# Kernel optimization log

Measured on AMD Instinct MI355X. Metric: run time of the kernel, lower is better.

The kernel has to match this reference:

```python
import jax, jax.numpy as jnp
import numpy as np

DIM = 2048; N_HEADS = 16; Q_RANK = 1536; KV_RANK = 192
NOPE = 128; ROPE = 64; QK_HD = NOPE + ROPE  # 192 == KV_RANK (required by k_norm/cache widths)
B = 2; S = 2048; MAX_SEQ = 2048
EPS = 1e-6
SCALE = QK_HD ** -0.5


def _rms(v, w):
    return v * jax.lax.rsqrt(jnp.mean(v * v, axis=-1, keepdims=True) + EPS) * w


def _rope(v, cos, sin):
    # v: [..., d] with interleaved (even, odd) pairs, cos/sin broadcastable to [..., d//2]
    vr = v.reshape(v.shape[:-1] + (-1, 2))
    a, b = vr[..., 0], vr[..., 1]
    return jnp.stack([a * cos - b * sin, a * sin + b * cos], axis=-1).reshape(v.shape)


def setup_inputs() -> dict:
    key = jax.random.key(0)
    ks = jax.random.split(key, 8)
    std = 0.02
    x = jax.random.normal(ks[0], (B, S, DIM), jnp.float32)
    # rotary tables: [S, ROPE//2, 2] = (cos, sin)
    t = jnp.arange(S, dtype=jnp.float32)
    inv = 1.0 / (10000.0 ** (jnp.arange(0, ROPE, 2, dtype=jnp.float32) / ROPE))
    ang = jnp.outer(t, inv)
    freqs_cis = jnp.stack([jnp.cos(ang), jnp.sin(ang)], axis=-1)
    mask = jnp.triu(jnp.full((S, S), -1e9, jnp.float32), k=1)  # causal additive mask
    c_kv_cache = jnp.zeros((B, MAX_SEQ, KV_RANK), jnp.float32)
    return {
        "x": x, "start_pos": 0, "freqs_cis": freqs_cis, "mask": mask,
        "c_kv_cache": c_kv_cache,
        "wqa_w": jax.random.normal(ks[1], (Q_RANK, DIM), jnp.float32) * std,
        "wqa_b": jnp.zeros((Q_RANK,), jnp.float32),
        "wqb_w": jax.random.normal(ks[2], (N_HEADS * QK_HD, Q_RANK), jnp.float32) * std,
        "wqb_b": jnp.zeros((N_HEADS * QK_HD,), jnp.float32),
        "q_norm_w": jnp.ones((Q_RANK,), jnp.float32),
        "wkva_w": jax.random.normal(ks[3], (QK_HD, DIM), jnp.float32) * std,
        "wkva_b": jnp.zeros((QK_HD,), jnp.float32),
        "k_norm_w": jnp.ones((KV_RANK,), jnp.float32),
        "wuk_w": jax.random.normal(ks[4], (NOPE, NOPE), jnp.float32) * std,
        "wuk_b": jnp.zeros((NOPE,), jnp.float32),
        "wuv_w": jax.random.normal(ks[5], (DIM, NOPE), jnp.float32) * std,
        "wuv_b": jnp.zeros((DIM,), jnp.float32),
    }


def reference(x, start_pos, freqs_cis, mask, c_kv_cache,
              wqa_w, wqa_b, wqb_w, wqb_b, q_norm_w,
              wkva_w, wkva_b, k_norm_w, wuk_w, wuk_b, wuv_w, wuv_b):
    bsz, seqlen, _ = x.shape
    end = start_pos + seqlen
    cos, sin = freqs_cis[..., 0], freqs_cis[..., 1]  # [seqlen, ROPE//2]

    # low-rank Q path: down-proj -> RMSNorm -> up-proj -> per-head split
    q = _rms(x @ wqa_w.T + wqa_b, q_norm_w)
    q = (q @ wqb_w.T + wqb_b).reshape(bsz, seqlen, N_HEADS, QK_HD)
    q_nope, q_pe = q[..., :NOPE], q[..., NOPE:]
    q_pe = _rope(q_pe, cos[None, :, None, :], sin[None, :, None, :])

    # latent KV path: project -> RMSNorm -> partial RoPE -> scatter into cache
    kv = _rms(x @ wkva_w.T + wkva_b, k_norm_w)  # [b, s, KV_RANK]
    k_pe = _rope(kv[..., NOPE:], cos[None, :, :], sin[None, :, :])
    kv = jnp.concatenate([kv[..., :NOPE], k_pe], axis=-1)
    cache = jax.lax.dynamic_update_slice(c_kv_cache, kv, (0, start_pos, 0))
    keys = cache[:bsz, :end]  # [b, t, KV_RANK]
    k_nope, k_rope = keys[..., :NOPE], keys[..., NOPE:]

    # absorbed attention: fold w_uk into the query side, attend in latent space
    q_abs = q_nope @ wuk_w.T + wuk_b  # [b, s, h, NOPE]
    scores = (jnp.einsum('bshd,btd->bsht', q_abs, k_nope)
              + jnp.einsum('bshr,btr->bsht', q_pe, k_rope)) * SCALE
    scores = scores + mask[None, :seqlen, None, :end]
    attn = jax.nn.softmax(scores, axis=-1)
    out = jnp.einsum('bsht,btd->bshd', attn, k_nope)  # latent values
    out = (out @ wuv_w.T + wuv_b).sum(axis=2)  # up-project values, merge heads -> [b, s, dim]
    return out
```

## Files before the change

kernel.cpp:

```cpp
#include <hip/hip_runtime.h>
#include <hip/hip_bf16.h>
#include <stdint.h>

#define NH     16
#define QRANK  1536
#define NOPE_  128
#define QKHD   192
#define B_     2
#define S_     2048
#define MAXSEQ 2048
#define EPS_   1e-6f
#define SCALE_ 0.07216878364870322f

typedef __attribute__((ext_vector_type(4))) float f32x4;
typedef __attribute__((ext_vector_type(8))) short short8;
typedef __attribute__((ext_vector_type(4))) short short4v;

__device__ inline short f2bf(float f){
  uint32_t u = __builtin_bit_cast(uint32_t, f);
  uint32_t r = (u + 0x7FFFu + ((u >> 16) & 1u)) >> 16;
  return (short)(uint16_t)r;
}
__device__ inline float bf2f(short s){
  uint32_t u = ((uint32_t)(uint16_t)s) << 16;
  return __builtin_bit_cast(float, u);
}
__device__ inline void gload16(const short* g, short* l){
  __builtin_amdgcn_global_load_lds((const __attribute__((address_space(1))) void*)g,
                                   (__attribute__((address_space(3))) void*)l, 16, 0, 0);
}

__global__ void k_f2b(const float* __restrict__ in, short* __restrict__ out, long n){
  long i = ((long)blockIdx.x * blockDim.x + threadIdx.x) * 4;
  long stride = (long)gridDim.x * blockDim.x * 4;
  for(; i < n; i += stride){
    float4 v = *reinterpret_cast<const float4*>(in + i);
    short4v o;
    o.x = f2bf(v.x); o.y = f2bf(v.y); o.z = f2bf(v.z); o.w = f2bf(v.w);
    *reinterpret_cast<short4v*>(out + i) = o;
  }
}

template<int BN, bool OUT_BF16>
__global__ __launch_bounds__(256)
void k_gemm97(const short* __restrict__ A, const short* __restrict__ Bm,
              const float* __restrict__ bias, float biasScale,
              void* __restrict__ Cp, int M, int N, int K, int ldc)
{
  constexpr int WN = BN / 2, FN = WN / 16;
  __shared__ short As[128 * 32];
  __shared__ short Bs[BN * 32];
  const int tid = threadIdx.x;
  const int l = tid & 63, w = tid >> 6;
  const int wr = w >> 1, wc = w & 1;
  const long m0 = (long)blockIdx.x * 128;
  const long n0 = (long)blockIdx.y * BN;
  const int lrow = l & 15, lk8 = (l >> 4) * 8;

  int ciA0 = (w*2 + 0)*64 + l, ciA1 = (w*2 + 1)*64 + l;
  const short* a0 = &A[(m0 + (ciA0 >> 2))*(long)K + (ciA0 & 3)*8];
  const short* a1 = &A[(m0 + (ciA1 >> 2))*(long)K + (ciA1 & 3)*8];
  short* lA0 = &As[(w*2 + 0)*512];
  short* lA1 = &As[(w*2 + 1)*512];

  const short* b0; const short* b1 = nullptr;
  short* lB0; short* lB1 = nullptr;
  if constexpr (BN == 128){
    int ciB0 = (w*2 + 0)*64 + l, ciB1 = (w*2 + 1)*64 + l;
    b0 = &Bm[(n0 + (ciB0 >> 2))*(long)K + (ciB0 & 3)*8];
    b1 = &Bm[(n0 + (ciB1 >> 2))*(long)K + (ciB1 & 3)*8];
    lB0 = &Bs[(w*2 + 0)*512];
    lB1 = &Bs[(w*2 + 1)*512];
  } else {
    int ciB = w*64 + l;
    b0 = &Bm[(n0 + (ciB >> 2))*(long)K + (ciB & 3)*8];
    lB0 = &Bs[w*512];
  }

  f32x4 acc[4][FN];
  #pragma unroll
  for(int m = 0; m < 4; m++)
    #pragma unroll
    for(int n = 0; n < FN; n++) acc[m][n] = (f32x4)0.0f;

  for(int kt = 0; kt < K; kt += 32){
    gload16(a0 + kt, lA0);
    gload16(a1 + kt, lA1);
    gload16(b0 + kt, lB0);
    if constexpr (BN == 128) gload16(b1 + kt, lB1);
    __syncthreads();
    short8 af[4], bfv[FN];
    #pragma unroll
    for(int m = 0; m < 4; m++)
      af[m] = *reinterpret_cast<const short8*>(&As[(wr*64 + m*16 + lrow)*32 + lk8]);
    #pragma unroll
    for(int n = 0; n < FN; n++)
      bfv[n] = *reinterpret_cast<const short8*>(&Bs[(wc*WN + n*16 + lrow)*32 + lk8]);
    #pragma unroll
    for(int m = 0; m < 4; m++)
      #pragma unroll
      for(int n = 0; n < FN; n++)
        acc[m][n] = __builtin_amdgcn_mfma_f32_16x16x32_bf16(af[m], bfv[n], acc[m][n], 0, 0, 0);
    __syncthreads();
  }
  #pragma unroll
  for(int m = 0; m < 4; m++){
    int row_l = wr*64 + m*16 + (l >> 4)*4;
    #pragma unroll
    for(int n = 0; n < FN; n++){
      int col = (int)n0 + wc*WN + n*16 + lrow;
      float bv = bias ? bias[col]*biasScale : 0.0f;
      #pragma unroll
      for(int r = 0; r < 4; r++){
        long row = m0 + row_l + r;
        float v = acc[m][n][r] + bv;
        if constexpr (OUT_BF16) ((short*)Cp)[row*(long)ldc + col] = f2bf(v);
        else                    ((float*)Cp)[row*(long)ldc + col] = v;
      }
    }
  }
}

template<int BN, bool OUT_BF16>
__global__ __launch_bounds__(256)
void k_gemm_bt(const short* __restrict__ A, const short* __restrict__ Bm,
               const float* __restrict__ bias, float biasScale,
               void* __restrict__ Cp, int M, int N, int K, int ldc)
{
  constexpr int BM = 128, PAD = 40;
  constexpr int WN = BN / 2, FN = WN / 16;
  __shared__ short As[BM * PAD];
  __shared__ short Bs[BN * PAD];
  const int tid = threadIdx.x;
  const int l = tid & 63, wid = tid >> 6;
  const int wr = wid >> 1, wc = wid & 1;
  const long m0 = (long)blockIdx.x * BM;
  const long n0 = (long)blockIdx.y * BN;
  const int lrow = l & 15, lk = (l >> 4) * 8;

  f32x4 acc[4][FN];
  for(int m = 0; m < 4; m++) for(int n = 0; n < FN; n++) acc[m][n] = (f32x4)0.0f;

  for(int kt = 0; kt < K; kt += 32){
    #pragma unroll
    for(int i = 0; i < BM/64; i++){
      int c = tid + 256*i;
      int row = c >> 2, ko = (c & 3) * 8;
      short8 v = *reinterpret_cast<const short8*>(&A[(m0 + row)*(long)K + kt + ko]);
      *reinterpret_cast<short8*>(&As[row*PAD + ko]) = v;
    }
    #pragma unroll
    for(int i = 0; i < BN/64; i++){
      int c = tid + 256*i;
      int row = c >> 2, ko = (c & 3) * 8;
      short8 v = *reinterpret_cast<const short8*>(&Bm[(n0 + row)*(long)K + kt + ko]);
      *reinterpret_cast<short8*>(&Bs[row*PAD + ko]) = v;
    }
    __syncthreads();
    short8 af[4], bfv[FN];
    #pragma unroll
    for(int m = 0; m < 4; m++)
      af[m] = *reinterpret_cast<const short8*>(&As[(wr*64 + m*16 + lrow)*PAD + lk]);
    #pragma unroll
    for(int n = 0; n < FN; n++)
      bfv[n] = *reinterpret_cast<const short8*>(&Bs[(wc*WN + n*16 + lrow)*PAD + lk]);
    #pragma unroll
    for(int m = 0; m < 4; m++)
      #pragma unroll
      for(int n = 0; n < FN; n++)
        acc[m][n] = __builtin_amdgcn_mfma_f32_16x16x32_bf16(af[m], bfv[n], acc[m][n], 0, 0, 0);
    __syncthreads();
  }
  #pragma unroll
  for(int m = 0; m < 4; m++){
    int row_l = wr*64 + m*16 + (l >> 4)*4;
    #pragma unroll
    for(int n = 0; n < FN; n++){
      int col = (int)n0 + wc*WN + n*16 + (l & 15);
      float bv = bias ? bias[col]*biasScale : 0.0f;
      #pragma unroll
      for(int r = 0; r < 4; r++){
        long row = m0 + row_l + r;
        float v = acc[m][n][r] + bv;
        if constexpr (OUT_BF16) ((short*)Cp)[row*(long)ldc + col] = f2bf(v);
        else                    ((float*)Cp)[row*(long)ldc + col] = v;
      }
    }
  }
}

__global__ __launch_bounds__(256)
void k_rms_q(const float* __restrict__ in, const float* __restrict__ w,
             short* __restrict__ out)
{
  const int row = blockIdx.x;
  const int tid = threadIdx.x;
  const float* p = in + (long)row * QRANK;
  float v[6]; float ss = 0.0f;
  #pragma unroll
  for(int i = 0; i < 6; i++){ v[i] = p[tid + 256*i]; ss += v[i]*v[i]; }
  #pragma unroll
  for(int off = 1; off < 64; off <<= 1) ss += __shfl_xor(ss, off);
  __shared__ float red[4];
  if((tid & 63) == 0) red[tid >> 6] = ss;
  __syncthreads();
  ss = red[0] + red[1] + red[2] + red[3];
  float scale = rsqrtf(ss / (float)QRANK + EPS_);
  #pragma unroll
  for(int i = 0; i < 6; i++){
    int c = tid + 256*i;
    out[(long)row*QRANK + c] = f2bf(v[i] * scale * w[c]);
  }
}

__global__ __launch_bounds__(256)
void k_qassemble(const short* __restrict__ q, const float* __restrict__ freqs,
                 short* __restrict__ qn, short* __restrict__ qfull)
{
  long idx = (long)blockIdx.x*256 + threadIdx.x;
  long hr = idx / 48; int r = (int)(idx % 48);
  long bs = hr >> 4; int h = (int)(hr & 15);
  int s = (int)(bs & (S_ - 1));
  if(r < 32){
    short4v v = *reinterpret_cast<const short4v*>(&q[bs*3072 + h*QKHD + r*4]);
    *reinterpret_cast<short4v*>(&qn[hr*128 + r*4]) = v;
  } else {
    int c = r - 32;
    short4v v = *reinterpret_cast<const short4v*>(&q[bs*3072 + h*QKHD + 128 + c*4]);
    float a0 = bf2f(v.x), b0 = bf2f(v.y), a1 = bf2f(v.z), b1 = bf2f(v.w);
    int p0 = s*32 + c*2, p1 = p0 + 1;
    float cs0 = freqs[p0*2], sn0 = freqs[p0*2 + 1];
    float cs1 = freqs[p1*2], sn1 = freqs[p1*2 + 1];
    short4v o;
    o.x = f2bf(a0*cs0 - b0*sn0); o.y = f2bf(a0*sn0 + b0*cs0);
    o.z = f2bf(a1*cs1 - b1*sn1); o.w = f2bf(a1*sn1 + b1*cs1);
    *reinterpret_cast<short4v*>(&qfull[hr*QKHD + 128 + c*4]) = o;
  }
}

__global__ __launch_bounds__(256)
void k_kvproc(const float* __restrict__ kvf, const float* __restrict__ w,
              const float* __restrict__ freqs, const float* __restrict__ cache,
              const int* __restrict__ sp_ptr, short* __restrict__ kf)
{
  int wid = threadIdx.x >> 6, l = threadIdx.x & 63;
  long row = (long)blockIdx.x*4 + wid;
  int b = (int)(row >> 11);
  int t = (int)(row & (MAXSEQ - 1));
  int sp = sp_ptr[0];
  int end = sp + S_;
  if(t < sp){
    const float* c = cache + row*QKHD;
    kf[row*QKHD + l]       = f2bf(c[l]);
    kf[row*QKHD + 64 + l]  = f2bf(c[64 + l]);
    kf[row*QKHD + 128 + l] = f2bf(c[128 + l]);
    return;
  }
  if(t >= end) return;
  int s = t - sp;
  const float* p = kvf + ((long)b*S_ + s)*QKHD;
  float v0 = p[l], v1 = p[64 + l], v2 = p[128 + l];
  float ss = v0*v0 + v1*v1 + v2*v2;
  #pragma unroll
  for(int off = 1; off < 64; off <<= 1) ss += __shfl_xor(ss, off);
  float scale = rsqrtf(ss / (float)QKHD + EPS_);
  float n0 = v0*scale*w[l], n1 = v1*scale*w[64 + l], n2 = v2*scale*w[128 + l];
  kf[row*QKHD + l]      = f2bf(n0);
  kf[row*QKHD + 64 + l] = f2bf(n1);
  int i = l >> 1;
  float cs = freqs[(s*32 + i)*2], sn = freqs[(s*32 + i)*2 + 1];
  float pv = __shfl_xor(n2, 1);
  float r = (l & 1) ? (pv*sn + n2*cs) : (n2*cs - pv*sn);
  kf[row*QKHD + 128 + l] = f2bf(r);
}

__global__ __launch_bounds__(256)
void k_vtrans(const short* __restrict__ kf, short* __restrict__ vt)
{
  __shared__ short T[32 * 132];
  const int b = blockIdx.y;
  const int t0 = blockIdx.x * 32;
  const int tid = threadIdx.x;
  #pragma unroll
  for(int i = 0; i < 4; i++){
    int c = tid + 256*i;
    int tr = c >> 5, dg = c & 31;
    short4v v = *reinterpret_cast<const short4v*>(&kf[((long)b*MAXSEQ + t0 + tr)*QKHD + dg*4]);
    *reinterpret_cast<short4v*>(&T[tr*132 + dg*4]) = v;
  }
  __syncthreads();
  #pragma unroll
  for(int i = 0; i < 4; i++){
    int c = tid + 256*i;
    int dr = c >> 3, tg = c & 7;
    short4v v;
    v.x = T[(tg*4 + 0)*132 + dr];
    v.y = T[(tg*4 + 1)*132 + dr];
    v.z = T[(tg*4 + 2)*132 + dr];
    v.w = T[(tg*4 + 3)*132 + dr];
    *reinterpret_cast<short4v*>(&vt[((long)b*128 + dr)*MAXSEQ + t0 + tg*4]) = v;
  }
}

__global__ __launch_bounds__(256, 3)
void k_attn5(const short* __restrict__ qfull, const short* __restrict__ kf,
             const short* __restrict__ vt, const int* __restrict__ sp_ptr,
             short* __restrict__ oh)
{
  __shared__ short Ks[64 * 192];
  __shared__ short Vs[128 * 64];
  __shared__ short Ps[4][16 * 68];
  const int tid = threadIdx.x;
  const int l = tid & 63, w = tid >> 6;
  const int lrow = l & 15, lhi = l >> 4;
  const int h = blockIdx.y, b = blockIdx.z;
  const int sp = sp_ptr[0];
  const long kbase = (long)b * MAXSEQ;
  const long vbase = (long)b * 128;

  short8 kreg[6], vreg[4];

  #pragma unroll 1
  for(int part = 0; part < 2; part++){
    const int tile = part ? (31 - (int)blockIdx.x) : (int)blockIdx.x;
    const int q0 = tile * 64;

    short8 qa[6];
    {
      int s = q0 + w*16 + lrow;
      const short* qp = qfull + (((long)b*S_ + s)*NH + h)*QKHD + lhi*8;
      #pragma unroll
      for(int ks = 0; ks < 6; ks++) qa[ks] = *reinterpret_cast<const short8*>(qp + ks*32);
    }
    f32x4 o[8];
    #pragma unroll
    for(int df = 0; df < 8; df++) o[df] = (f32x4)0.0f;
    float mrun[4], lrun[4];
    #pragma unroll
    for(int i = 0; i < 4; i++){ mrun[i] = -1e30f; lrun[i] = 0.0f; }

    int hi = q0 + 64 + sp;
    int nt = (hi + 63) >> 6; if(nt > (MAXSEQ >> 6)) nt = MAXSEQ >> 6;

    {
      #pragma unroll
      for(int i = 0; i < 6; i++){
        int cid = tid + 256*i;  int r = cid/24, c = cid%24;
        kreg[i] = *reinterpret_cast<const short8*>(&kf[(kbase + r)*QKHD + c*8]);
      }
      #pragma unroll
      for(int i = 0; i < 4; i++){
        int cid = tid + 256*i;  int r = cid >> 3, c = cid & 7;
        vreg[i] = *reinterpret_cast<const short8*>(&vt[(vbase + r)*MAXSEQ + c*8]);
      }
      #pragma unroll
      for(int i = 0; i < 6; i++){
        int cid = tid + 256*i;  int r = cid/24, c = cid%24;
        *reinterpret_cast<short8*>(&Ks[r*192 + (c ^ (r & 7))*8]) = kreg[i];
      }
      #pragma unroll
      for(int i = 0; i < 4; i++){
        int cid = tid + 256*i;  int r = cid >> 3, c = cid & 7;
        *reinterpret_cast<short8*>(&Vs[r*64 + (c ^ (r & 7))*8]) = vreg[i];
      }
    }
    __syncthreads();

    for(int t0 = 0; t0 < nt; t0++){
      const int T0 = t0 * 64;
      if(t0 + 1 < nt){
        const int Tn = T0 + 64;
        #pragma unroll
        for(int i = 0; i < 6; i++){
          int cid = tid + 256*i;  int r = cid/24, c = cid%24;
          kreg[i] = *reinterpret_cast<const short8*>(&kf[(kbase + Tn + r)*QKHD + c*8]);
        }
        #pragma unroll
        for(int i = 0; i < 4; i++){
          int cid = tid + 256*i;  int r = cid >> 3, c = cid & 7;
          vreg[i] = *reinterpret_cast<const short8*>(&vt[(vbase + r)*MAXSEQ + Tn + c*8]);
        }
      }
      f32x4 sc[4];
      #pragma unroll
      for(int tf = 0; tf < 4; tf++) sc[tf] = (f32x4)0.0f;
      #pragma unroll
      for(int ks = 0; ks < 6; ks++){
        #pragma unroll
        for(int tf = 0; tf < 4; tf++){
          int krow = tf*16 + lrow;
          int cs = (ks*4 + lhi) ^ (lrow & 7);
          short8 bfr = *reinterpret_cast<const short8*>(&Ks[krow*192 + cs*8]);
          sc[tf] = __builtin_amdgcn_mfma_f32_16x16x32_bf16(qa[ks], bfr, sc[tf], 0, 0, 0);
        }
      }
      const bool needmask = (T0 + 63 > q0 + w*16 + sp);
      #pragma unroll
      for(int rr = 0; rr < 4; rr++){
        int q = q0 + w*16 + lhi*4 + rr;
        float s0 = sc[0][rr]*SCALE_, s1 = sc[1][rr]*SCALE_;
        float s2 = sc[2][rr]*SCALE_, s3 = sc[3][rr]*SCALE_;
        if(needmask){
          int t = T0 + lrow;
          if(t      > q + sp) s0 = -1e30f;
          if(t + 16 > q + sp) s1 = -1e30f;
          if(t + 32 > q + sp) s2 = -1e30f;
          if(t + 48 > q + sp) s3 = -1e30f;
        }
        float mx = fmaxf(fmaxf(s0, s1), fmaxf(s2, s3));
        #pragma unroll
        for(int off = 1; off < 16; off <<= 1) mx = fmaxf(mx, __shfl_xor(mx, off));
        if(mx > mrun[rr] + 8.0f){
          float corr = __expf(mrun[rr] - mx);
          lrun[rr] *= corr;
          #pragma unroll
          for(int df = 0; df < 8; df++) o[df][rr] *= corr;
          mrun[rr] = mx;
        }
        float p0 = __expf(s0 - mrun[rr]), p1 = __expf(s1 - mrun[rr]);
        float p2 = __expf(s2 - mrun[rr]), p3 = __expf(s3 - mrun[rr]);
        float psum = (p0 + p1) + (p2 + p3);
        #pragma unroll
        for(int off = 1; off < 16; off <<= 1) psum += __shfl_xor(psum, off);
        lrun[rr] += psum;
        int prow = lhi*4 + rr;
        Ps[w][prow*68 + lrow]      = f2bf(p0);
        Ps[w][prow*68 + 16 + lrow] = f2bf(p1);
        Ps[w][prow*68 + 32 + lrow] = f2bf(p2);
        Ps[w][prow*68 + 48 + lrow] = f2bf(p3);
      }
      short8 pa[2];
      #pragma unroll
      for(int kc = 0; kc < 2; kc++)
        pa[kc] = *reinterpret_cast<const short8*>(&Ps[w][lrow*68 + kc*32 + lhi*8]);
      #pragma unroll
      for(int df = 0; df < 8; df++){
        #pragma unroll
        for(int kc = 0; kc < 2; kc++){
          int vrow = df*16 + lrow;
          int cs = (kc*4 + lhi) ^ (lrow & 7);
          short8 vfr = *reinterpret_cast<const short8*>(&Vs[vrow*64 + cs*8]);
          o[df] = __builtin_amdgcn_mfma_f32_16x16x32_bf16(pa[kc], vfr, o[df], 0, 0, 0);
        }
      }
      __syncthreads();
      if(t0 + 1 < nt){
        #pragma unroll
        for(int i = 0; i < 6; i++){
          int cid = tid + 256*i;  int r = cid/24, c = cid%24;
          *reinterpret_cast<short8*>(&Ks[r*192 + (c ^ (r & 7))*8]) = kreg[i];
        }
        #pragma unroll
        for(int i = 0; i < 4; i++){
          int cid = tid + 256*i;  int r = cid >> 3, c = cid & 7;
          *reinterpret_cast<short8*>(&Vs[r*64 + (c ^ (r & 7))*8]) = vreg[i];
        }
        __syncthreads();
      }
    }
    #pragma unroll
    for(int rr = 0; rr < 4; rr++){
      int s = q0 + w*16 + lhi*4 + rr;
      float inv = 1.0f / lrun[rr];
      #pragma unroll
      for(int df = 0; df < 8; df++)
        oh[(((long)b*S_ + s)*NH + h)*128 + df*16 + lrow] = f2bf(o[df][rr] * inv);
    }
  }
}

__global__ __launch_bounds__(256)
void k_redheads(const short* __restrict__ ohp, short* __restrict__ hs){
  long idx = (long)blockIdx.x*256 + threadIdx.x;
  long row = idx >> 5; int d4 = (int)(idx & 31);
  float a0 = 0, a1 = 0, a2 = 0, a3 = 0;
  #pragma unroll
  for(int h = 0; h < NH; h++){
    short4v v = *reinterpret_cast<const short4v*>(&ohp[(row*NH + h)*128 + d4*4]);
    a0 += bf2f(v.x); a1 += bf2f(v.y); a2 += bf2f(v.z); a3 += bf2f(v.w);
  }
  short4v o; o.x = f2bf(a0); o.y = f2bf(a1); o.z = f2bf(a2); o.w = f2bf(a3);
  *reinterpret_cast<short4v*>(&hs[row*128 + d4*4]) = o;
}

static constexpr size_t OFF_X16   = 0;
static constexpr size_t OFF_WQA   = 16777216;
static constexpr size_t OFF_WQB   = 23068672;
static constexpr size_t OFF_WKV   = 32505856;
static constexpr size_t OFF_WUK   = 33292288;
static constexpr size_t OFF_WUV   = 33325056;
static constexpr size_t OFF_QNORM = 33849344;
static constexpr size_t OFF_QFULL = 46432256;
static constexpr size_t OFF_KFULL = 71598080;
static constexpr size_t OFF_HSUM  = 73170944;
static constexpr size_t OFF_SCR   = 74219520;
static constexpr size_t OFF_QA    = OFF_SCR;
static constexpr size_t OFF_Q16   = OFF_SCR;
static constexpr size_t OFF_QN    = OFF_SCR + 25165824;
static constexpr size_t OFF_KVF   = OFF_SCR + 41943040;
static constexpr size_t OFF_OH    = OFF_SCR;
static constexpr size_t OFF_VT    = OFF_SCR + 25165824;

extern "C" void kernel_launch(void* const* d_in, const int* in_sizes, int n_in,
                              void* d_out, int out_size, void* d_ws, size_t ws_size,
                              hipStream_t stream)
{
  const float* x      = (const float*)d_in[0];
  const int*   sp     = (const int*)  d_in[1];
  const float* freqs  = (const float*)d_in[2];
  const float* cache  = (const float*)d_in[4];
  const float* wqa_w  = (const float*)d_in[5];
  const float* wqa_b  = (const float*)d_in[6];
  const float* wqb_w  = (const float*)d_in[7];
  const float* wqb_b  = (const float*)d_in[8];
  const float* qnw    = (const float*)d_in[9];
  const float* wkva_w = (const float*)d_in[10];
  const float* wkva_b = (const float*)d_in[11];
  const float* knw    = (const float*)d_in[12];
  const float* wuk_w  = (const float*)d_in[13];
  const float* wuk_b  = (const float*)d_in[14];
  const float* wuv_w  = (const float*)d_in[15];
  const float* wuv_b  = (const float*)d_in[16];

  char* ws = (char*)d_ws;
  short* X16   = (short*)(ws + OFF_X16);
  short* WQA16 = (short*)(ws + OFF_WQA);
  short* WQB16 = (short*)(ws + OFF_WQB);
  short* WKV16 = (short*)(ws + OFF_WKV);
  short* WUK16 = (short*)(ws + OFF_WUK);
  short* WUV16 = (short*)(ws + OFF_WUV);
  short* QNORM = (short*)(ws + OFF_QNORM);
  short* QFULL = (short*)(ws + OFF_QFULL);
  short* KFULL = (short*)(ws + OFF_KFULL);
  short* HSUM  = (short*)(ws + OFF_HSUM);
  float* QA    = (float*)(ws + OFF_QA);
  short* Q16   = (short*)(ws + OFF_Q16);
  short* QN16  = (short*)(ws + OFF_QN);
  float* KVF   = (float*)(ws + OFF_KVF);
  short* OH16  = (short*)(ws + OFF_OH);
  short* VT16  = (short*)(ws + OFF_VT);

  auto cvt = [&](const float* src, short* dst, long n){
    long blocks = (n/4 + 255) / 256; if(blocks > 2048) blocks = 2048;
    k_f2b<<<(int)blocks, 256, 0, stream>>>(src, dst, n);
  };
  cvt(x,      X16,   (long)B_*S_*2048);
  cvt(wqa_w,  WQA16, (long)QRANK*2048);
  cvt(wqb_w,  WQB16, (long)NH*QKHD*QRANK);
  cvt(wkva_w, WKV16, (long)QKHD*2048);
  cvt(wuk_w,  WUK16, (long)NOPE_*NOPE_);
  cvt(wuv_w,  WUV16, (long)2048*NOPE_);

  k_gemm97<64,false><<<dim3(32,24), 256, 0, stream>>>(X16, WQA16, wqa_b, 1.0f, QA, 4096, QRANK, 2048, QRANK);
  k_rms_q<<<4096, 256, 0, stream>>>(QA, qnw, QNORM);
  k_gemm97<128,true><<<dim3(32,24), 256, 0, stream>>>(QNORM, WQB16, wqb_b, 1.0f, Q16, 4096, NH*QKHD, QRANK, NH*QKHD);
  k_qassemble<<<12288, 256, 0, stream>>>(Q16, freqs, QN16, QFULL);
  k_gemm97<128,true><<<dim3(512,1), 256, 0, stream>>>(QN16, WUK16, wuk_b, 1.0f, QFULL, 65536, 128, 128, QKHD);
  k_gemm_bt<64,false><<<dim3(32,3), 256, 0, stream>>>(X16, WKV16, wkva_b, 1.0f, KVF, 4096, QKHD, 2048, QKHD);
  k_kvproc<<<1024, 256, 0, stream>>>(KVF, knw, freqs, cache, sp, KFULL);
  k_vtrans<<<dim3(64,2), 256, 0, stream>>>(KFULL, VT16);
  k_attn5<<<dim3(16,16,2), 256, 0, stream>>>(QFULL, KFULL, VT16, sp, OH16);
  k_redheads<<<512, 256, 0, stream>>>(OH16, HSUM);
  k_gemm97<64,false><<<dim3(32,32), 256, 0, stream>>>(HSUM, WUV16, wuv_b, 16.0f, (float*)d_out, 4096, 2048, NOPE_, 2048);
}
```

Baseline: 513.7 us.

## Merge Q-down and KV-down GEMMs; restructure attention grid with direct V loads

Concatenates wqa and wkva weights so a single GEMM produces both the Q latent and KV latent outputs, with the biases now added in the RMSNorm kernels. This removes the separate small, poorly occupied KV projection GEMM. The attention kernel now handles one query tile per block, with a heavy-first tile ordering across 1024 blocks in place of paired tiles. It drops the V shared-memory staging and reads V fragments directly from global memory, which frees LDS and allows 4 blocks per CU. The trade-off is uncoalesced V reads from global memory through cache.

```diff
diff --git a/kernel.cpp b/kernel.cpp
--- a/kernel.cpp
+++ b/kernel.cpp
@@ -6,6 +6,7 @@
 #define QRANK  1536
 #define NOPE_  128
 #define QKHD   192
+#define NMERGE 1728
 #define B_     2
 #define S_     2048
 #define MAXSEQ 2048
@@ -121,84 +122,20 @@
   }
 }
 
-template<int BN, bool OUT_BF16>
-__global__ __launch_bounds__(256)
-void k_gemm_bt(const short* __restrict__ A, const short* __restrict__ Bm,
-               const float* __restrict__ bias, float biasScale,
-               void* __restrict__ Cp, int M, int N, int K, int ldc)
-{
-  constexpr int BM = 128, PAD = 40;
-  constexpr int WN = BN / 2, FN = WN / 16;
-  __shared__ short As[BM * PAD];
-  __shared__ short Bs[BN * PAD];
-  const int tid = threadIdx.x;
-  const int l = tid & 63, wid = tid >> 6;
-  const int wr = wid >> 1, wc = wid & 1;
-  const long m0 = (long)blockIdx.x * BM;
-  const long n0 = (long)blockIdx.y * BN;
-  const int lrow = l & 15, lk = (l >> 4) * 8;
-
-  f32x4 acc[4][FN];
-  for(int m = 0; m < 4; m++) for(int n = 0; n < FN; n++) acc[m][n] = (f32x4)0.0f;
-
-  for(int kt = 0; kt < K; kt += 32){
-    #pragma unroll
-    for(int i = 0; i < BM/64; i++){
-      int c = tid + 256*i;
-      int row = c >> 2, ko = (c & 3) * 8;
-      short8 v = *reinterpret_cast<const short8*>(&A[(m0 + row)*(long)K + kt + ko]);
-      *reinterpret_cast<short8*>(&As[row*PAD + ko]) = v;
-    }
-    #pragma unroll
-    for(int i = 0; i < BN/64; i++){
-      int c = tid + 256*i;
-      int row = c >> 2, ko = (c & 3) * 8;
-      short8 v = *reinterpret_cast<const short8*>(&Bm[(n0 + row)*(long)K + kt + ko]);
-      *reinterpret_cast<short8*>(&Bs[row*PAD + ko]) = v;
-    }
-    __syncthreads();
-    short8 af[4], bfv[FN];
-    #pragma unroll
-    for(int m = 0; m < 4; m++)
-      af[m] = *reinterpret_cast<const short8*>(&As[(wr*64 + m*16 + lrow)*PAD + lk]);
-    #pragma unroll
-    for(int n = 0; n < FN; n++)
-      bfv[n] = *reinterpret_cast<const short8*>(&Bs[(wc*WN + n*16 + lrow)*PAD + lk]);
-    #pragma unroll
-    for(int m = 0; m < 4; m++)
-      #pragma unroll
-      for(int n = 0; n < FN; n++)
-        acc[m][n] = __builtin_amdgcn_mfma_f32_16x16x32_bf16(af[m], bfv[n], acc[m][n], 0, 0, 0);
-    __syncthreads();
-  }
-  #pragma unroll
-  for(int m = 0; m < 4; m++){
-    int row_l = wr*64 + m*16 + (l >> 4)*4;
-    #pragma unroll
-    for(int n = 0; n < FN; n++){
-      int col = (int)n0 + wc*WN + n*16 + (l & 15);
-      float bv = bias ? bias[col]*biasScale : 0.0f;
-      #pragma unroll
-      for(int r = 0; r < 4; r++){
-        long row = m0 + row_l + r;
-        float v = acc[m][n][r] + bv;
-        if constexpr (OUT_BF16) ((short*)Cp)[row*(long)ldc + col] = f2bf(v);
-        else                    ((float*)Cp)[row*(long)ldc + col] = v;
-      }
-    }
-  }
-}
-
-__global__ __launch_bounds__(256)
-void k_rms_q(const float* __restrict__ in, const float* __restrict__ w,
-             short* __restrict__ out)
+__global__ __launch_bounds__(256)
+void k_rms_q(const float* __restrict__ in, const float* __restrict__ bias,
+             const float* __restrict__ w, short* __restrict__ out)
 {
   const int row = blockIdx.x;
   const int tid = threadIdx.x;
-  const float* p = in + (long)row * QRANK;
+  const float* p = in + (long)row * NMERGE;
   float v[6]; float ss = 0.0f;
   #pragma unroll
-  for(int i = 0; i < 6; i++){ v[i] = p[tid + 256*i]; ss += v[i]*v[i]; }
+  for(int i = 0; i < 6; i++){
+    int c = tid + 256*i;
+    v[i] = p[c] + bias[c];
+    ss += v[i]*v[i];
+  }
   #pragma unroll
   for(int off = 1; off < 64; off <<= 1) ss += __shfl_xor(ss, off);
   __shared__ float red[4];
@@ -239,9 +176,10 @@
 }
 
 __global__ __launch_bounds__(256)
-void k_kvproc(const float* __restrict__ kvf, const float* __restrict__ w,
-              const float* __restrict__ freqs, const float* __restrict__ cache,
-              const int* __restrict__ sp_ptr, short* __restrict__ kf)
+void k_kvproc(const float* __restrict__ kvf, const float* __restrict__ kvb,
+              const float* __restrict__ w, const float* __restrict__ freqs,
+              const float* __restrict__ cache, const int* __restrict__ sp_ptr,
+              short* __restrict__ kf)
 {
   int wid = threadIdx.x >> 6, l = threadIdx.x & 63;
   long row = (long)blockIdx.x*4 + wid;
@@ -258,8 +196,10 @@
   }
   if(t >= end) return;
   int s = t - sp;
-  const float* p = kvf + ((long)b*S_ + s)*QKHD;
-  float v0 = p[l], v1 = p[64 + l], v2 = p[128 + l];
+  const float* p = kvf + ((long)b*S_ + s)*NMERGE;
+  float v0 = p[l] + kvb[l];
+  float v1 = p[64 + l] + kvb[64 + l];
+  float v2 = p[128 + l] + kvb[128 + l];
   float ss = v0*v0 + v1*v1 + v2*v2;
   #pragma unroll
   for(int off = 1; off < 64; off <<= 1) ss += __shfl_xor(ss, off);
@@ -302,170 +242,146 @@
   }
 }
 
-__global__ __launch_bounds__(256, 3)
-void k_attn5(const short* __restrict__ qfull, const short* __restrict__ kf,
+__global__ __launch_bounds__(256, 4)
+void k_attn6(const short* __restrict__ qfull, const short* __restrict__ kf,
              const short* __restrict__ vt, const int* __restrict__ sp_ptr,
              short* __restrict__ oh)
 {
   __shared__ short Ks[64 * 192];
-  __shared__ short Vs[128 * 64];
   __shared__ short Ps[4][16 * 68];
   const int tid = threadIdx.x;
   const int l = tid & 63, w = tid >> 6;
   const int lrow = l & 15, lhi = l >> 4;
-  const int h = blockIdx.y, b = blockIdx.z;
+  const int bid = blockIdx.x;
+  const int g = bid >> 8, kk = (bid >> 5) & 7, hb = bid & 31;
+  const int tile = (g < 2) ? (31 - 8*g - kk) : (8*(3 - g) + kk);
+  const int h = hb & 15, b = hb >> 4;
   const int sp = sp_ptr[0];
   const long kbase = (long)b * MAXSEQ;
   const long vbase = (long)b * 128;
-
-  short8 kreg[6], vreg[4];
-
-  #pragma unroll 1
-  for(int part = 0; part < 2; part++){
-    const int tile = part ? (31 - (int)blockIdx.x) : (int)blockIdx.x;
-    const int q0 = tile * 64;
-
-    short8 qa[6];
-    {
-      int s = q0 + w*16 + lrow;
-      const short* qp = qfull + (((long)b*S_ + s)*NH + h)*QKHD + lhi*8;
-      #pragma unroll
-      for(int ks = 0; ks < 6; ks++) qa[ks] = *reinterpret_cast<const short8*>(qp + ks*32);
-    }
-    f32x4 o[8];
-    #pragma unroll
-    for(int df = 0; df < 8; df++) o[df] = (f32x4)0.0f;
-    float mrun[4], lrun[4];
-    #pragma unroll
-    for(int i = 0; i < 4; i++){ mrun[i] = -1e30f; lrun[i] = 0.0f; }
-
-    int hi = q0 + 64 + sp;
-    int nt = (hi + 63) >> 6; if(nt > (MAXSEQ >> 6)) nt = MAXSEQ >> 6;
-
-    {
+  const int q0 = tile * 64;
+
+  short8 kreg[6];
+
+  short8 qa[6];
+  {
+    int s = q0 + w*16 + lrow;
+    const short* qp = qfull + (((long)b*S_ + s)*NH + h)*QKHD + lhi*8;
+    #pragma unroll
+    for(int ks = 0; ks < 6; ks++) qa[ks] = *reinterpret_cast<const short8*>(qp + ks*32);
+  }
+  f32x4 o[8];
+  #pragma unroll
+  for(int df = 0; df < 8; df++) o[df] = (f32x4)0.0f;
+  float mrun[4], lrun[4];
+  #pragma unroll
+  for(int i = 0; i < 4; i++){ mrun[i] = -1e30f; lrun[i] = 0.0f; }
+
+  int hi = q0 + 64 + sp;
+  int nt = (hi + 63) >> 6; if(nt > (MAXSEQ >> 6)) nt = MAXSEQ >> 6;
+
+  {
+    #pragma unroll
+    for(int i = 0; i < 6; i++){
+      int cid = tid + 256*i;  int r = cid/24, c = cid%24;
+      kreg[i] = *reinterpret_cast<const short8*>(&kf[(kbase + r)*QKHD + c*8]);
+    }
+    #pragma unroll
+    for(int i = 0; i < 6; i++){
+      int cid = tid + 256*i;  int r = cid/24, c = cid%24;
+      *reinterpret_cast<short8*>(&Ks[r*192 + (c ^ (r & 7))*8]) = kreg[i];
+    }
+  }
+  __syncthreads();
+
+  for(int t0 = 0; t0 < nt; t0++){
+    const int T0 = t0 * 64;
+    if(t0 + 1 < nt){
+      const int Tn = T0 + 64;
       #pragma unroll
       for(int i = 0; i < 6; i++){
         int cid = tid + 256*i;  int r = cid/24, c = cid%24;
-        kreg[i] = *reinterpret_cast<const short8*>(&kf[(kbase + r)*QKHD + c*8]);
-      }
-      #pragma unroll
-      for(int i = 0; i < 4; i++){
-        int cid = tid + 256*i;  int r = cid >> 3, c = cid & 7;
-        vreg[i] = *reinterpret_cast<const short8*>(&vt[(vbase + r)*MAXSEQ + c*8]);
-      }
+        kreg[i] = *reinterpret_cast<const short8*>(&kf[(kbase + Tn + r)*QKHD + c*8]);
+      }
+    }
+    f32x4 sc[4];
+    #pragma unroll
+    for(int tf = 0; tf < 4; tf++) sc[tf] = (f32x4)0.0f;
+    #pragma unroll
+    for(int ks = 0; ks < 6; ks++){
+      #pragma unroll
+      for(int tf = 0; tf < 4; tf++){
+        int krow = tf*16 + lrow;
+        int cs = (ks*4 + lhi) ^ (lrow & 7);
+        short8 bfr = *reinterpret_cast<const short8*>(&Ks[krow*192 + cs*8]);
+        sc[tf] = __builtin_amdgcn_mfma_f32_16x16x32_bf16(qa[ks], bfr, sc[tf], 0, 0, 0);
+      }
+    }
+    const bool needmask = (T0 + 63 > q0 + w*16 + sp);
+    #pragma unroll
+    for(int rr = 0; rr < 4; rr++){
+      int q = q0 + w*16 + lhi*4 + rr;
+      float s0 = sc[0][rr]*SCALE_, s1 = sc[1][rr]*SCALE_;
+      float s2 = sc[2][rr]*SCALE_, s3 = sc[3][rr]*SCALE_;
+      if(needmask){
+        int t = T0 + lrow;
+        if(t      > q + sp) s0 = -1e30f;
+        if(t + 16 > q + sp) s1 = -1e30f;
+        if(t + 32 > q + sp) s2 = -1e30f;
+        if(t + 48 > q + sp) s3 = -1e30f;
+      }
+      float mx = fmaxf(fmaxf(s0, s1), fmaxf(s2, s3));
+      #pragma unroll
+      for(int off = 1; off < 16; off <<= 1) mx = fmaxf(mx, __shfl_xor(mx, off));
+      if(mx > mrun[rr] + 8.0f){
+        float corr = __expf(mrun[rr] - mx);
+        lrun[rr] *= corr;
+        #pragma unroll
+        for(int df = 0; df < 8; df++) o[df][rr] *= corr;
+        mrun[rr] = mx;
+      }
+      float p0 = __expf(s0 - mrun[rr]), p1 = __expf(s1 - mrun[rr]);
+      float p2 = __expf(s2 - mrun[rr]), p3 = __expf(s3 - mrun[rr]);
+      float psum = (p0 + p1) + (p2 + p3);
+      #pragma unroll
+      for(int off = 1; off < 16; off <<= 1) psum += __shfl_xor(psum, off);
+      lrun[rr] += psum;
+      int prow = lhi*4 + rr;
+      Ps[w][prow*68 + lrow]      = f2bf(p0);
+      Ps[w][prow*68 + 16 + lrow] = f2bf(p1);
+      Ps[w][prow*68 + 32 + lrow] = f2bf(p2);
+      Ps[w][prow*68 + 48 + lrow] = f2bf(p3);
+    }
+    short8 pa[2];
+    #pragma unroll
+    for(int kc = 0; kc < 2; kc++)
+      pa[kc] = *reinterpret_cast<const short8*>(&Ps[w][lrow*68 + kc*32 + lhi*8]);
+    #pragma unroll
+    for(int df = 0; df < 8; df++){
+      #pragma unroll
+      for(int kc = 0; kc < 2; kc++){
+        short8 vfr = *reinterpret_cast<const short8*>(
+            &vt[(vbase + df*16 + lrow)*MAXSEQ + T0 + kc*32 + lhi*8]);
+        o[df] = __builtin_amdgcn_mfma_f32_16x16x32_bf16(pa[kc], vfr, o[df], 0, 0, 0);
+      }
+    }
+    __syncthreads();
+    if(t0 + 1 < nt){
       #pragma unroll
       for(int i = 0; i < 6; i++){
         int cid = tid + 256*i;  int r = cid/24, c = cid%24;
         *reinterpret_cast<short8*>(&Ks[r*192 + (c ^ (r & 7))*8]) = kreg[i];
       }
-      #pragma unroll
-      for(int i = 0; i < 4; i++){
-        int cid = tid + 256*i;  int r = cid >> 3, c = cid & 7;
-        *reinterpret_cast<short8*>(&Vs[r*64 + (c ^ (r & 7))*8]) = vreg[i];
-      }
-    }
-    __syncthreads();
-
-    for(int t0 = 0; t0 < nt; t0++){
-      const int T0 = t0 * 64;
-      if(t0 + 1 < nt){
-        const int Tn = T0 + 64;
-        #pragma unroll
-        for(int i = 0; i < 6; i++){
-          int cid = tid + 256*i;  int r = cid/24, c = cid%24;
-          kreg[i] = *reinterpret_cast<const short8*>(&kf[(kbase + Tn + r)*QKHD + c*8]);
-        }
-        #pragma unroll
-        for(int i = 0; i < 4; i++){
-          int cid = tid + 256*i;  int r = cid >> 3, c = cid & 7;
-          vreg[i] = *reinterpret_cast<const short8*>(&vt[(vbase + r)*MAXSEQ + Tn + c*8]);
-        }
-      }
-      f32x4 sc[4];
-      #pragma unroll
-      for(int tf = 0; tf < 4; tf++) sc[tf] = (f32x4)0.0f;
-      #pragma unroll
-      for(int ks = 0; ks < 6; ks++){
-        #pragma unroll
-        for(int tf = 0; tf < 4; tf++){
-          int krow = tf*16 + lrow;
-          int cs = (ks*4 + lhi) ^ (lrow & 7);
-          short8 bfr = *reinterpret_cast<const short8*>(&Ks[krow*192 + cs*8]);
-          sc[tf] = __builtin_amdgcn_mfma_f32_16x16x32_bf16(qa[ks], bfr, sc[tf], 0, 0, 0);
-        }
-      }
-      const bool needmask = (T0 + 63 > q0 + w*16 + sp);
-      #pragma unroll
-      for(int rr = 0; rr < 4; rr++){
-        int q = q0 + w*16 + lhi*4 + rr;
-        float s0 = sc[0][rr]*SCALE_, s1 = sc[1][rr]*SCALE_;
-        float s2 = sc[2][rr]*SCALE_, s3 = sc[3][rr]*SCALE_;
-        if(needmask){
-          int t = T0 + lrow;
-          if(t      > q + sp) s0 = -1e30f;
-          if(t + 16 > q + sp) s1 = -1e30f;
-          if(t + 32 > q + sp) s2 = -1e30f;
-          if(t + 48 > q + sp) s3 = -1e30f;
-        }
-        float mx = fmaxf(fmaxf(s0, s1), fmaxf(s2, s3));
-        #pragma unroll
-        for(int off = 1; off < 16; off <<= 1) mx = fmaxf(mx, __shfl_xor(mx, off));
-        if(mx > mrun[rr] + 8.0f){
-          float corr = __expf(mrun[rr] - mx);
-          lrun[rr] *= corr;
-          #pragma unroll
-          for(int df = 0; df < 8; df++) o[df][rr] *= corr;
-          mrun[rr] = mx;
-        }
-        float p0 = __expf(s0 - mrun[rr]), p1 = __expf(s1 - mrun[rr]);
-        float p2 = __expf(s2 - mrun[rr]), p3 = __expf(s3 - mrun[rr]);
-        float psum = (p0 + p1) + (p2 + p3);
-        #pragma unroll
-        for(int off = 1; off < 16; off <<= 1) psum += __shfl_xor(psum, off);
-        lrun[rr] += psum;
-        int prow = lhi*4 + rr;
-        Ps[w][prow*68 + lrow]      = f2bf(p0);
-        Ps[w][prow*68 + 16 + lrow] = f2bf(p1);
-        Ps[w][prow*68 + 32 + lrow] = f2bf(p2);
-        Ps[w][prow*68 + 48 + lrow] = f2bf(p3);
-      }
-      short8 pa[2];
-      #pragma unroll
-      for(int kc = 0; kc < 2; kc++)
-        pa[kc] = *reinterpret_cast<const short8*>(&Ps[w][lrow*68 + kc*32 + lhi*8]);
-      #pragma unroll
-      for(int df = 0; df < 8; df++){
-        #pragma unroll
-        for(int kc = 0; kc < 2; kc++){
-          int vrow = df*16 + lrow;
-          int cs = (kc*4 + lhi) ^ (lrow & 7);
-          short8 vfr = *reinterpret_cast<const short8*>(&Vs[vrow*64 + cs*8]);
-          o[df] = __builtin_amdgcn_mfma_f32_16x16x32_bf16(pa[kc], vfr, o[df], 0, 0, 0);
-        }
-      }
       __syncthreads();
-      if(t0 + 1 < nt){
-        #pragma unroll
-        for(int i = 0; i < 6; i++){
-          int cid = tid + 256*i;  int r = cid/24, c = cid%24;
-          *reinterpret_cast<short8*>(&Ks[r*192 + (c ^ (r & 7))*8]) = kreg[i];
-        }
-        #pragma unroll
-        for(int i = 0; i < 4; i++){
-          int cid = tid + 256*i;  int r = cid >> 3, c = cid & 7;
-          *reinterpret_cast<short8*>(&Vs[r*64 + (c ^ (r & 7))*8]) = vreg[i];
-        }
-        __syncthreads();
-      }
-    }
-    #pragma unroll
-    for(int rr = 0; rr < 4; rr++){
-      int s = q0 + w*16 + lhi*4 + rr;
-      float inv = 1.0f / lrun[rr];
-      #pragma unroll
-      for(int df = 0; df < 8; df++)
-        oh[(((long)b*S_ + s)*NH + h)*128 + df*16 + lrow] = f2bf(o[df][rr] * inv);
-    }
+    }
+  }
+  #pragma unroll
+  for(int rr = 0; rr < 4; rr++){
+    int s = q0 + w*16 + lhi*4 + rr;
+    float inv = 1.0f / lrun[rr];
+    #pragma unroll
+    for(int df = 0; df < 8; df++)
+      oh[(((long)b*S_ + s)*NH + h)*128 + df*16 + lrow] = f2bf(o[df][rr] * inv);
   }
 }
 
@@ -484,9 +400,8 @@
 }
 
 static constexpr size_t OFF_X16   = 0;
-static constexpr size_t OFF_WQA   = 16777216;
-static constexpr size_t OFF_WQB   = 23068672;
-static constexpr size_t OFF_WKV   = 32505856;
+static constexpr size_t OFF_WQAKV = 16777216;
+static constexpr size_t OFF_WQB   = 23855104;
 static constexpr size_t OFF_WUK   = 33292288;
 static constexpr size_t OFF_WUV   = 33325056;
 static constexpr size_t OFF_QNORM = 33849344;
@@ -494,12 +409,11 @@
 static constexpr size_t OFF_KFULL = 71598080;
 static constexpr size_t OFF_HSUM  = 73170944;
 static constexpr size_t OFF_SCR   = 74219520;
-static constexpr size_t OFF_QA    = OFF_SCR;
+static constexpr size_t OFF_QAKV  = OFF_SCR;
 static constexpr size_t OFF_Q16   = OFF_SCR;
 static constexpr size_t OFF_QN    = OFF_SCR + 25165824;
-static constexpr size_t OFF_KVF   = OFF_SCR + 41943040;
 static constexpr size_t OFF_OH    = OFF_SCR;
-static constexpr size_t OFF_VT    = OFF_SCR + 25165824;
+static constexpr size_t OFF_VT    = OFF_SCR + 41943040;
 
 extern "C" void kernel_launch(void* const* d_in, const int* in_sizes, int n_in,
                               void* d_out, int out_size, void* d_ws, size_t ws_size,
@@ -524,19 +438,17 @@
 
   char* ws = (char*)d_ws;
   short* X16   = (short*)(ws + OFF_X16);
-  short* WQA16 = (short*)(ws + OFF_WQA);
+  short* WQAKV = (short*)(ws + OFF_WQAKV);
   short* WQB16 = (short*)(ws + OFF_WQB);
-  short* WKV16 = (short*)(ws + OFF_WKV);
   short* WUK16 = (short*)(ws + OFF_WUK);
   short* WUV16 = (short*)(ws + OFF_WUV);
   short* QNORM = (short*)(ws + OFF_QNORM);
   short* QFULL = (short*)(ws + OFF_QFULL);
   short* KFULL = (short*)(ws + OFF_KFULL);
   short* HSUM  = (short*)(ws + OFF_HSUM);
-  float* QA    = (float*)(ws + OFF_QA);
+  float* QAKV  = (float*)(ws + OFF_QAKV);
   short* Q16   = (short*)(ws + OFF_Q16);
   short* QN16  = (short*)(ws + OFF_QN);
-  float* KVF   = (float*)(ws + OFF_KVF);
   short* OH16  = (short*)(ws + OFF_OH);
   short* VT16  = (short*)(ws + OFF_VT);
 
@@ -545,21 +457,20 @@
     k_f2b<<<(int)blocks, 256, 0, stream>>>(src, dst, n);
   };
   cvt(x,      X16,   (long)B_*S_*2048);
-  cvt(wqa_w,  WQA16, (long)QRANK*2048);
+  cvt(wqa_w,  WQAKV, (long)QRANK*2048);
+  cvt(wkva_w, WQAKV + (long)QRANK*2048, (long)QKHD*2048);
   cvt(wqb_w,  WQB16, (long)NH*QKHD*QRANK);
-  cvt(wkva_w, WKV16, (long)QKHD*2048);
   cvt(wuk_w,  WUK16, (long)NOPE_*NOPE_);
   cvt(wuv_w,  WUV16, (long)2048*NOPE_);
 
-  k_gemm97<64,false><<<dim3(32,24), 256, 0, stream>>>(X16, WQA16, wqa_b, 1.0f, QA, 4096, QRANK, 2048, QRANK);
-  k_rms_q<<<4096, 256, 0, stream>>>(QA, qnw, QNORM);
+  k_gemm97<64,false><<<dim3(32,27), 256, 0, stream>>>(X16, WQAKV, nullptr, 0.0f, QAKV, 4096, NMERGE, 2048, NMERGE);
+  k_rms_q<<<4096, 256, 0, stream>>>(QAKV, wqa_b, qnw, QNORM);
+  k_kvproc<<<1024, 256, 0, stream>>>(QAKV + QRANK, wkva_b, knw, freqs, cache, sp, KFULL);
   k_gemm97<128,true><<<dim3(32,24), 256, 0, stream>>>(QNORM, WQB16, wqb_b, 1.0f, Q16, 4096, NH*QKHD, QRANK, NH*QKHD);
   k_qassemble<<<12288, 256, 0, stream>>>(Q16, freqs, QN16, QFULL);
   k_gemm97<128,true><<<dim3(512,1), 256, 0, stream>>>(QN16, WUK16, wuk_b, 1.0f, QFULL, 65536, 128, 128, QKHD);
-  k_gemm_bt<64,false><<<dim3(32,3), 256, 0, stream>>>(X16, WKV16, wkva_b, 1.0f, KVF, 4096, QKHD, 2048, QKHD);
-  k_kvproc<<<1024, 256, 0, stream>>>(KVF, knw, freqs, cache, sp, KFULL);
   k_vtrans<<<dim3(64,2), 256, 0, stream>>>(KFULL, VT16);
-  k_attn5<<<dim3(16,16,2), 256, 0, stream>>>(QFULL, KFULL, VT16, sp, OH16);
+  k_attn6<<<1024, 256, 0, stream>>>(QFULL, KFULL, VT16, sp, OH16);
   k_redheads<<<512, 256, 0, stream>>>(OH16, HSUM);
   k_gemm97<64,false><<<dim3(32,32), 256, 0, stream>>>(HSUM, WUV16, wuv_b, 16.0f, (float*)d_out, 4096, 2048, NOPE_, 2048);
 }
```

Result: slower. 579.5 us (+12.8%).
